# Kernel tuning notes

Measured on AMD Instinct MI355X. Metric: run time of the kernel, lower is better.

Reference implementation:

```python
import jax, jax.numpy as jnp
import numpy as np

B, S, D = 4, 2048, 1024
D_K, D_V = 1024, 1024


def setup_inputs() -> dict:
    key = jax.random.key(0)
    ks = jax.random.split(key, 9)
    s = 1.0 / np.sqrt(D)
    return {
        "q_in": jax.random.normal(ks[0], (B, S, D), jnp.float32),
        "k_in": jax.random.normal(ks[1], (B, S, D), jnp.float32),
        "v_in": jax.random.normal(ks[2], (B, S, D), jnp.float32),
        "Wq": jax.random.normal(ks[3], (D, D_K), jnp.float32) * s,
        "bq": jnp.zeros((D_K,), jnp.float32),
        "Wk": jax.random.normal(ks[4], (D, D_K), jnp.float32) * s,
        "bk": jnp.zeros((D_K,), jnp.float32),
        "Wv": jax.random.normal(ks[5], (D, D_V), jnp.float32) * s,
        "bv": jnp.zeros((D_V,), jnp.float32),
    }


def reference(q_in, k_in, v_in, Wq, bq, Wk, bk, Wv, bv):
    q = jnp.einsum("bsd,dk->bsk", q_in, Wq) + bq  # [B,S,d_k]
    k = jnp.einsum("bsd,dk->bsk", k_in, Wk) + bk  # [B,S,d_k]
    v = jnp.einsum("bsd,dv->bsv", v_in, Wv) + bv  # [B,S,d_v]
    scores = jnp.einsum("bqk,bsk->bqs", q, k) / jnp.sqrt(jnp.float32(D_K))
    attn = jax.nn.softmax(scores, axis=-1)  # [B,S,S]
    return jnp.einsum("bqs,bsv->bqv", attn, v)
```

## Files before the change

kernel.cpp:

```cpp
#include <hip/hip_runtime.h>
#include <stdint.h>

#define B_  4
#define S_  2048
#define D_  1024
#define DK_ 1024
#define DV_ 1024

typedef __attribute__((ext_vector_type(8)))  short short8;
typedef __attribute__((ext_vector_type(16))) float floatx16;

#define ASYNC16(gsrc, ldst)                                                        \
  __builtin_amdgcn_global_load_lds(                                                \
      (const __attribute__((address_space(1))) unsigned int*)(gsrc),               \
      (__attribute__((address_space(3))) unsigned int*)(ldst), 16, 0, 0)

#define WAITVM(N) asm volatile("s_waitcnt vmcnt(" #N ")" ::: "memory")

__device__ __forceinline__ unsigned short f2bf(float f) {
  union { float f; uint32_t u; } v; v.f = f;
  uint32_t r = v.u + 0x7fffu + ((v.u >> 16) & 1u);
  return (unsigned short)(r >> 16);
}

__global__ __launch_bounds__(256)
void prep(const float* __restrict__ q, const float* __restrict__ k, const float* __restrict__ v,
          const float* __restrict__ W0, const float* __restrict__ W1, const float* __restrict__ W2,
          unsigned short* __restrict__ qkv, unsigned short* __restrict__ WT) {
  const int bid = blockIdx.x, tid = threadIdx.x;
  if (bid < 12288) {
    const int t  = bid >> 12;
    const int cb = bid & 4095;
    const float* in = (t == 0) ? q : (t == 1) ? k : v;
    unsigned short* o = qkv + (long)t * ((long)B_ * S_ * D_);
    const int i0 = cb * 512 + tid;
    float4 v0 = ((const float4*)in)[i0];
    float4 v1 = ((const float4*)in)[i0 + 256];
    ushort4 u0, u1;
    u0.x = f2bf(v0.x); u0.y = f2bf(v0.y); u0.z = f2bf(v0.z); u0.w = f2bf(v0.w);
    u1.x = f2bf(v1.x); u1.y = f2bf(v1.y); u1.z = f2bf(v1.z); u1.w = f2bf(v1.w);
    ((ushort4*)o)[i0] = u0;
    ((ushort4*)o)[i0 + 256] = u1;
  } else {
    const int b2 = bid - 12288;
    const int w  = b2 >> 10;
    const int tl = b2 & 1023;
    const float* in = (w == 0) ? W0 : (w == 1) ? W1 : W2;
    unsigned short* o = WT + (long)w * D_ * DK_;
    __shared__ float tile[32][33];
    const int bx = (tl & 31) * 32, by = (tl >> 5) * 32;
    const int tx = tid & 31, ty = tid >> 5;
    for (int r = ty; r < 32; r += 8)
      tile[r][tx] = in[(long)(by + r) * DK_ + bx + tx];
    __syncthreads();
    for (int r = ty; r < 32; r += 8)
      o[(long)(bx + r) * D_ + by + tx] = f2bf(tile[tx][r]);
  }
}

__device__ __forceinline__ void storeC(float* p, float v)          { *p = v; }
__device__ __forceinline__ void storeC(unsigned short* p, float v) { *p = f2bf(v); }

template <typename OutT, int NOUT, int MODE, int KSPL>
__global__ __launch_bounds__(512, 2)
void gemm_bt256(const unsigned short* __restrict__ A0, const unsigned short* __restrict__ A1,
                const unsigned short* __restrict__ A2, const unsigned short* __restrict__ Bm,
                OutT* __restrict__ C0, OutT* __restrict__ C1, OutT* __restrict__ C2,
                const float* __restrict__ b0, const float* __restrict__ b1,
                const float* __restrict__ b2, float* __restrict__ rowsum,
                int N, int K, int lda, int ldb, long sA, long sB, long sC, float scale) {
  __shared__ __align__(16) unsigned short As[3][256 * 32];
  __shared__ __align__(16) unsigned short Bs[3][256 * 32];
  __shared__ float invs[256];
  const int tid  = threadIdx.x;
  const int lane = tid & 63, wave = tid >> 6;
  const int wm = (wave >> 2) * 128;
  const int wn = (wave & 3) * 64;
  const int lm = lane & 31;
  const int hi = lane >> 5;

  const int gx = gridDim.x, gy = gridDim.y;
  const int T  = gx * gy * (int)gridDim.z;
  const int l  = blockIdx.x + gx * (blockIdx.y + gy * blockIdx.z);
  const int l2 = (l & 7) * (T >> 3) + (l >> 3);
  const int bxi = l2 % gx;
  const int byi = (l2 / gx) % gy;
  const int bzi = l2 / (gx * gy);

  const int  kh = (KSPL > 1) ? (bzi & (KSPL - 1)) : 0;
  const long zb = (KSPL > 1) ? (bzi >> 1) : bzi;
  const int m0  = byi * 256;
  const int n0g = bxi * 256;

  const unsigned short* A = A0;
  OutT* C = C0;
  const float* bias = b0;
  int n0 = n0g, sel = 0;
  if (NOUT == 3) {
    sel = n0g >> 10;
    n0 = n0g & 1023;
    if (sel == 1)      { A = A1; C = C1; bias = b1; }
    else if (sel == 2) { A = A2; C = C2; bias = b2; }
  }
  A += zb * sA + (long)kh * K;
  const unsigned short* Bp = Bm + zb * sB + (long)kh * K;
  C += zb * sC;

  const int rr = lane >> 2;
  const int cc = (((lane & 3) ^ ((lane >> 3) & 3)) * 8);
  const unsigned short* gA0 = A  + (long)(m0  + 32 * wave + rr) * lda + cc;
  const unsigned short* gA1 = gA0 + 16 * (long)lda;
  const unsigned short* gB0 = Bp + (long)(n0g + 32 * wave + rr) * ldb + cc;
  const unsigned short* gB1 = gB0 + 16 * (long)ldb;
  const int la0 = wave * 1024, la1 = wave * 1024 + 512;

  floatx16 acc[4][2] = {};
  const int sw = (lm >> 1) & 3;

  const int nt = K >> 5;

  ASYNC16(gA0, &As[0][la0]); ASYNC16(gA1, &As[0][la1]);
  ASYNC16(gB0, &Bs[0][la0]); ASYNC16(gB1, &Bs[0][la1]);
  gA0 += 32; gA1 += 32; gB0 += 32; gB1 += 32;
  ASYNC16(gA0, &As[1][la0]); ASYNC16(gA1, &As[1][la1]);
  ASYNC16(gB0, &Bs[1][la0]); ASYNC16(gB1, &Bs[1][la1]);
  gA0 += 32; gA1 += 32; gB0 += 32; gB1 += 32;
  WAITVM(4);
  __builtin_amdgcn_s_barrier();

  int bc = 0;
  for (int t = 0; t < nt; t++) {
    const int bs = (bc + 2 >= 3) ? bc - 1 : bc + 2;
    const bool pre = (t + 2 < nt);

    short8 af[2][2], bf[2][2];
#pragma unroll
    for (int i = 0; i < 2; i++)
#pragma unroll
      for (int s = 0; s < 2; s++)
        af[i][s] = *(const short8*)&As[bc][(wm + i * 32 + lm) * 32 + (((s * 2 + hi) ^ sw) * 8)];
#pragma unroll
    for (int j = 0; j < 2; j++)
#pragma unroll
      for (int s = 0; s < 2; s++)
        bf[j][s] = *(const short8*)&Bs[bc][(wn + j * 32 + lm) * 32 + (((s * 2 + hi) ^ sw) * 8)];
    if (pre) {
      ASYNC16(gA0, &As[bs][la0]); ASYNC16(gA1, &As[bs][la1]);
      gA0 += 32; gA1 += 32;
    }
    __builtin_amdgcn_s_barrier();
    asm volatile("s_waitcnt lgkmcnt(0)" ::: "memory");
    __builtin_amdgcn_s_setprio(1);
#pragma unroll
    for (int s = 0; s < 2; s++)
#pragma unroll
      for (int i = 0; i < 2; i++)
#pragma unroll
        for (int j = 0; j < 2; j++)
          acc[i][j] = __builtin_amdgcn_mfma_f32_32x32x16_bf16(af[i][s], bf[j][s], acc[i][j], 0, 0, 0);
    __builtin_amdgcn_s_setprio(0);
    __builtin_amdgcn_s_barrier();

    short8 af2[2][2];
#pragma unroll
    for (int i = 0; i < 2; i++)
#pragma unroll
      for (int s = 0; s < 2; s++)
        af2[i][s] = *(const short8*)&As[bc][(wm + (2 + i) * 32 + lm) * 32 + (((s * 2 + hi) ^ sw) * 8)];
    if (pre) {
      ASYNC16(gB0, &Bs[bs][la0]); ASYNC16(gB1, &Bs[bs][la1]);
      gB0 += 32; gB1 += 32;
    }
    __builtin_amdgcn_s_barrier();
    asm volatile("s_waitcnt lgkmcnt(0)" ::: "memory");
    __builtin_amdgcn_s_setprio(1);
#pragma unroll
    for (int s = 0; s < 2; s++)
#pragma unroll
      for (int i = 0; i < 2; i++)
#pragma unroll
        for (int j = 0; j < 2; j++)
          acc[2 + i][j] = __builtin_amdgcn_mfma_f32_32x32x16_bf16(af2[i][s], bf[j][s], acc[2 + i][j], 0, 0, 0);
    __builtin_amdgcn_s_setprio(0);
    if (pre) { WAITVM(4); } else { WAITVM(0); }
    __builtin_amdgcn_s_barrier();
    bc = (bc == 2) ? 0 : bc + 1;
  }

  if (MODE == 2 || MODE == 3) {
    __syncthreads();
    if (tid < 256) invs[tid] = 1.0f / rowsum[zb * S_ + m0 + tid];
    __syncthreads();
  }

  if (NOUT == 3 && sel == 2) {
    unsigned short* Vt = (unsigned short*)C;
    const int b = m0 >> 11;
    const int sbase = (m0 & 2047);
#pragma unroll
    for (int i = 0; i < 4; i++) {
      const int srowb = sbase + wm + i * 32 + (hi << 2);
#pragma unroll
      for (int j = 0; j < 2; j++) {
        const int col = n0 + wn + j * 32 + lm;
        const float bv = bias[col];
        unsigned short* vp = Vt + ((long)b * DV_ + col) * S_ + srowb;
#pragma unroll
        for (int g = 0; g < 4; g++) {
          ushort4 u;
          u.x = f2bf(acc[i][j][4 * g + 0] + bv);
          u.y = f2bf(acc[i][j][4 * g + 1] + bv);
          u.z = f2bf(acc[i][j][4 * g + 2] + bv);
          u.w = f2bf(acc[i][j][4 * g + 3] + bv);
          *(ushort4*)(vp + 8 * g) = u;
        }
      }
    }
  } else if (MODE == 1) {
#pragma unroll
    for (int i = 0; i < 4; i++) {
#pragma unroll
      for (int r = 0; r < 16; r++) {
        const int row = m0 + wm + i * 32 + (r & 3) + ((r >> 2) << 3) + (hi << 2);
        float sum2 = 0.f;
#pragma unroll
        for (int j = 0; j < 2; j++) {
          const int col = n0 + wn + j * 32 + lm;
          float e = __expf(acc[i][j][r] * scale);
          storeC(C + (long)row * N + col, e);
          sum2 += e;
        }
#pragma unroll
        for (int msk = 1; msk < 32; msk <<= 1) sum2 += __shfl_xor(sum2, msk, 64);
        if ((lane & 31) == 0) atomicAdd(&rowsum[zb * S_ + row], sum2);
      }
    }
  } else {
#pragma unroll
    for (int i = 0; i < 4; i++) {
#pragma unroll
      for (int j = 0; j < 2; j++) {
        const int col = n0 + wn + j * 32 + lm;
        const float bv = bias ? bias[col] : 0.f;
#pragma unroll
        for (int r = 0; r < 16; r++) {
          const int rl = wm + i * 32 + (r & 3) + ((r >> 2) << 3) + (hi << 2);
          float val = acc[i][j][r] * scale + bv;
          if (MODE == 3) {
            atomicAdd((float*)(C + (long)(m0 + rl) * N + col), val * invs[rl]);
          } else {
            if (MODE == 2) val *= invs[rl];
            storeC(C + (long)(m0 + rl) * N + col, val);
          }
        }
      }
    }
  }
}

extern "C" void kernel_launch(void* const* d_in, const int* in_sizes, int n_in,
                              void* d_out, int out_size, void* d_ws, size_t ws_size,
                              hipStream_t stream) {
  const float* q_in = (const float*)d_in[0];
  const float* k_in = (const float*)d_in[1];
  const float* v_in = (const float*)d_in[2];
  const float* Wq   = (const float*)d_in[3];
  const float* bq   = (const float*)d_in[4];
  const float* Wk   = (const float*)d_in[5];
  const float* bk   = (const float*)d_in[6];
  const float* Wv   = (const float*)d_in[7];
  const float* bv   = (const float*)d_in[8];
  float* out = (float*)d_out;

  char* ws = (char*)d_ws;
  const long nX = (long)B_ * S_ * D_;
  const long nW = (long)D_ * DK_;
  unsigned short* qb  = (unsigned short*)(ws);
  unsigned short* kb  = qb + nX;
  unsigned short* vb  = kb + nX;
  unsigned short* WqT = vb + nX;
  unsigned short* Qb  = WqT + 3 * nW;
  unsigned short* Kb  = Qb + nX;
  unsigned short* Vt  = Kb + nX;
  float*          rowsum = (float*)(Vt + nX);
  unsigned short* U   = (unsigned short*)ws;

  dim3 blk(256), blk5(512);

  hipMemsetAsync(rowsum, 0, (size_t)B_ * S_ * sizeof(float), stream);
  hipMemsetAsync(out, 0, (size_t)B_ * S_ * DV_ * sizeof(float), stream);

  {
    dim3 g(12288 + 3072);
    prep<<<g, blk, 0, stream>>>(q_in, k_in, v_in, Wq, Wk, Wv, qb, WqT);
  }
  {
    dim3 g(3 * DK_ / 256, (B_ * S_) / 256, 1);
    gemm_bt256<unsigned short, 3, 0, 1><<<g, blk5, 0, stream>>>(
        qb, kb, vb, WqT, Qb, Kb, Vt, bq, bk, bv, nullptr,
        DK_, D_, D_, D_, 0, 0, 0, 1.f);
  }
  {
    dim3 g(S_ / 256, S_ / 256, B_);
    gemm_bt256<unsigned short, 1, 1, 1><<<g, blk5, 0, stream>>>(
        Qb, nullptr, nullptr, Kb, U, nullptr, nullptr, nullptr, nullptr, nullptr, rowsum,
        S_, DK_, DK_, DK_, (long)S_ * DK_, (long)S_ * DK_, (long)S_ * S_, 0.03125f);
  }
  {
    dim3 g(DV_ / 256, S_ / 256, B_ * 2);
    gemm_bt256<float, 1, 3, 2><<<g, blk5, 0, stream>>>(
        U, nullptr, nullptr, Vt, out, nullptr, nullptr, nullptr, nullptr, nullptr, rowsum,
        DV_, S_ / 2, S_, S_, (long)S_ * S_, (long)DV_ * S_, (long)S_ * DV_, 1.f);
  }
}
```

Before: 374.0 us.

## Replace atomic row sums and split-K atomics with separate reduction and combine kernels

The QK^T kernel no longer uses shuffle reductions and atomicAdd to build softmax row sums. A separate kernel now computes the sums from the stored bf16 exponentials. The split-K PV GEMM writes its two halves to separate buffers with plain stores instead of float atomics into a zeroed output. A combine kernel then adds the halves and normalizes by the row sum. This removes two memsets and atomic traffic, but adds two extra launches, extra passes over U and the output, and the row sums are now computed from bf16-rounded values.

```diff
diff --git a/kernel.cpp b/kernel.cpp
--- a/kernel.cpp
+++ b/kernel.cpp
@@ -21,6 +21,11 @@
   union { float f; uint32_t u; } v; v.f = f;
   uint32_t r = v.u + 0x7fffu + ((v.u >> 16) & 1u);
   return (unsigned short)(r >> 16);
+}
+
+__device__ __forceinline__ float bf2f(unsigned short u) {
+  union { uint32_t u; float f; } v; v.u = ((uint32_t)u) << 16;
+  return v.f;
 }
 
 __global__ __launch_bounds__(256)
@@ -61,17 +66,46 @@
 __device__ __forceinline__ void storeC(float* p, float v)          { *p = v; }
 __device__ __forceinline__ void storeC(unsigned short* p, float v) { *p = f2bf(v); }
 
+__global__ __launch_bounds__(256)
+void rowsumk(const unsigned short* __restrict__ U, float* __restrict__ rowsum) {
+  const int w    = (blockIdx.x << 2) + (threadIdx.x >> 6);
+  const int lane = threadIdx.x & 63;
+  const unsigned short* row = U + (long)w * S_;
+  float s = 0.f;
+#pragma unroll
+  for (int it = 0; it < 4; it++) {
+    short8 v = *(const short8*)(row + it * 512 + lane * 8);
+#pragma unroll
+    for (int e = 0; e < 8; e++) s += bf2f((unsigned short)v[e]);
+  }
+#pragma unroll
+  for (int m = 1; m < 64; m <<= 1) s += __shfl_xor(s, m, 64);
+  if (lane == 0) rowsum[w] = s;
+}
+
+__global__ __launch_bounds__(256)
+void combine(float* __restrict__ out, const float* __restrict__ P,
+             const float* __restrict__ rowsum) {
+  const long k = (long)blockIdx.x * 256 + threadIdx.x;
+  float4 a = ((const float4*)out)[k];
+  float4 b = ((const float4*)P)[k];
+  const float inv = 1.0f / rowsum[k >> 8];
+  float4 o;
+  o.x = (a.x + b.x) * inv; o.y = (a.y + b.y) * inv;
+  o.z = (a.z + b.z) * inv; o.w = (a.w + b.w) * inv;
+  ((float4*)out)[k] = o;
+}
+
 template <typename OutT, int NOUT, int MODE, int KSPL>
 __global__ __launch_bounds__(512, 2)
 void gemm_bt256(const unsigned short* __restrict__ A0, const unsigned short* __restrict__ A1,
                 const unsigned short* __restrict__ A2, const unsigned short* __restrict__ Bm,
                 OutT* __restrict__ C0, OutT* __restrict__ C1, OutT* __restrict__ C2,
                 const float* __restrict__ b0, const float* __restrict__ b1,
-                const float* __restrict__ b2, float* __restrict__ rowsum,
+                const float* __restrict__ b2,
                 int N, int K, int lda, int ldb, long sA, long sB, long sC, float scale) {
   __shared__ __align__(16) unsigned short As[3][256 * 32];
   __shared__ __align__(16) unsigned short Bs[3][256 * 32];
-  __shared__ float invs[256];
   const int tid  = threadIdx.x;
   const int lane = tid & 63, wave = tid >> 6;
   const int wm = (wave >> 2) * 128;
@@ -102,6 +136,7 @@
     if (sel == 1)      { A = A1; C = C1; bias = b1; }
     else if (sel == 2) { A = A2; C = C2; bias = b2; }
   }
+  if (KSPL > 1 && kh) C = C1;
   A += zb * sA + (long)kh * K;
   const unsigned short* Bp = Bm + zb * sB + (long)kh * K;
   C += zb * sC;
@@ -185,12 +220,6 @@
     if (pre) { WAITVM(4); } else { WAITVM(0); }
     __builtin_amdgcn_s_barrier();
     bc = (bc == 2) ? 0 : bc + 1;
-  }
-
-  if (MODE == 2 || MODE == 3) {
-    __syncthreads();
-    if (tid < 256) invs[tid] = 1.0f / rowsum[zb * S_ + m0 + tid];
-    __syncthreads();
   }
 
   if (NOUT == 3 && sel == 2) {
@@ -220,19 +249,13 @@
 #pragma unroll
     for (int i = 0; i < 4; i++) {
 #pragma unroll
-      for (int r = 0; r < 16; r++) {
-        const int row = m0 + wm + i * 32 + (r & 3) + ((r >> 2) << 3) + (hi << 2);
-        float sum2 = 0.f;
-#pragma unroll
-        for (int j = 0; j < 2; j++) {
-          const int col = n0 + wn + j * 32 + lm;
-          float e = __expf(acc[i][j][r] * scale);
-          storeC(C + (long)row * N + col, e);
-          sum2 += e;
+      for (int j = 0; j < 2; j++) {
+        const int col = n0 + wn + j * 32 + lm;
+#pragma unroll
+        for (int r = 0; r < 16; r++) {
+          const int row = m0 + wm + i * 32 + (r & 3) + ((r >> 2) << 3) + (hi << 2);
+          storeC(C + (long)row * N + col, __expf(acc[i][j][r] * scale));
         }
-#pragma unroll
-        for (int msk = 1; msk < 32; msk <<= 1) sum2 += __shfl_xor(sum2, msk, 64);
-        if ((lane & 31) == 0) atomicAdd(&rowsum[zb * S_ + row], sum2);
       }
     }
   } else {
@@ -245,13 +268,7 @@
 #pragma unroll
         for (int r = 0; r < 16; r++) {
           const int rl = wm + i * 32 + (r & 3) + ((r >> 2) << 3) + (hi << 2);
-          float val = acc[i][j][r] * scale + bv;
-          if (MODE == 3) {
-            atomicAdd((float*)(C + (long)(m0 + rl) * N + col), val * invs[rl]);
-          } else {
-            if (MODE == 2) val *= invs[rl];
-            storeC(C + (long)(m0 + rl) * N + col, val);
-          }
+          storeC(C + (long)(m0 + rl) * N + col, acc[i][j][r] * scale + bv);
         }
       }
     }
@@ -284,11 +301,9 @@
   unsigned short* Vt  = Kb + nX;
   float*          rowsum = (float*)(Vt + nX);
   unsigned short* U   = (unsigned short*)ws;
+  float*          P   = (float*)Qb;
 
   dim3 blk(256), blk5(512);
-
-  hipMemsetAsync(rowsum, 0, (size_t)B_ * S_ * sizeof(float), stream);
-  hipMemsetAsync(out, 0, (size_t)B_ * S_ * DV_ * sizeof(float), stream);
 
   {
     dim3 g(12288 + 3072);
@@ -297,19 +312,27 @@
   {
     dim3 g(3 * DK_ / 256, (B_ * S_) / 256, 1);
     gemm_bt256<unsigned short, 3, 0, 1><<<g, blk5, 0, stream>>>(
-        qb, kb, vb, WqT, Qb, Kb, Vt, bq, bk, bv, nullptr,
+        qb, kb, vb, WqT, Qb, Kb, Vt, bq, bk, bv,
         DK_, D_, D_, D_, 0, 0, 0, 1.f);
   }
   {
     dim3 g(S_ / 256, S_ / 256, B_);
     gemm_bt256<unsigned short, 1, 1, 1><<<g, blk5, 0, stream>>>(
-        Qb, nullptr, nullptr, Kb, U, nullptr, nullptr, nullptr, nullptr, nullptr, rowsum,
+        Qb, nullptr, nullptr, Kb, U, nullptr, nullptr, nullptr, nullptr, nullptr,
         S_, DK_, DK_, DK_, (long)S_ * DK_, (long)S_ * DK_, (long)S_ * S_, 0.03125f);
   }
   {
+    dim3 g((B_ * S_) / 4);
+    rowsumk<<<g, blk, 0, stream>>>(U, rowsum);
+  }
+  {
     dim3 g(DV_ / 256, S_ / 256, B_ * 2);
-    gemm_bt256<float, 1, 3, 2><<<g, blk5, 0, stream>>>(
-        U, nullptr, nullptr, Vt, out, nullptr, nullptr, nullptr, nullptr, nullptr, rowsum,
+    gemm_bt256<float, 1, 0, 2><<<g, blk5, 0, stream>>>(
+        U, nullptr, nullptr, Vt, out, P, nullptr, nullptr, nullptr, nullptr,
         DV_, S_ / 2, S_, S_, (long)S_ * S_, (long)DV_ * S_, (long)S_ * DV_, 1.f);
   }
-}
+  {
+    dim3 g((B_ * S_ * DV_) / 4 / 256);
+    combine<<<g, blk, 0, stream>>>(out, P, rowsum);
+  }
+}
```

Result: faster. 340.4 us (-9.0%).

## Replace atomics with partial buffers plus combine kernel, deepen LDS pipeline to four stages

Applied to the files above, without the earlier changes.

The softmax row sums are now written as per-column-block partials instead of atomically added, and the split-K PV GEMM writes its two halves to separate buffers (out and P) with plain stores instead of float atomics. A new combine kernel adds the halves, reduces the partial row sums and applies the normalisation. This removes both memsets and the atomic traffic. The GEMM pipeline also grows from three to four LDS buffers with deeper prefetch, which raises LDS use and may lower occupancy, and the extra combine pass rereads the output.

```diff
diff --git a/kernel.cpp b/kernel.cpp
--- a/kernel.cpp
+++ b/kernel.cpp
@@ -61,17 +61,39 @@
 __device__ __forceinline__ void storeC(float* p, float v)          { *p = v; }
 __device__ __forceinline__ void storeC(unsigned short* p, float v) { *p = f2bf(v); }
 
+__global__ __launch_bounds__(256)
+void combine(float* __restrict__ out, const float* __restrict__ P,
+             const float* __restrict__ rsp) {
+  __shared__ float sinv;
+  const int row = blockIdx.x;
+  const int tid = threadIdx.x;
+  if (tid < 32) {
+    float s = rsp[(long)tid * (B_ * S_) + row];
+#pragma unroll
+    for (int m = 1; m < 32; m <<= 1) s += __shfl_xor(s, m, 64);
+    if (tid == 0) sinv = 1.0f / s;
+  }
+  __syncthreads();
+  const float inv = sinv;
+  const long k = (long)row * 256 + tid;
+  float4 a = ((const float4*)out)[k];
+  float4 b = ((const float4*)P)[k];
+  float4 o;
+  o.x = (a.x + b.x) * inv; o.y = (a.y + b.y) * inv;
+  o.z = (a.z + b.z) * inv; o.w = (a.w + b.w) * inv;
+  ((float4*)out)[k] = o;
+}
+
 template <typename OutT, int NOUT, int MODE, int KSPL>
 __global__ __launch_bounds__(512, 2)
 void gemm_bt256(const unsigned short* __restrict__ A0, const unsigned short* __restrict__ A1,
                 const unsigned short* __restrict__ A2, const unsigned short* __restrict__ Bm,
                 OutT* __restrict__ C0, OutT* __restrict__ C1, OutT* __restrict__ C2,
                 const float* __restrict__ b0, const float* __restrict__ b1,
-                const float* __restrict__ b2, float* __restrict__ rowsum,
+                const float* __restrict__ b2, float* __restrict__ rsp,
                 int N, int K, int lda, int ldb, long sA, long sB, long sC, float scale) {
-  __shared__ __align__(16) unsigned short As[3][256 * 32];
-  __shared__ __align__(16) unsigned short Bs[3][256 * 32];
-  __shared__ float invs[256];
+  __shared__ __align__(16) unsigned short As[4][256 * 32];
+  __shared__ __align__(16) unsigned short Bs[4][256 * 32];
   const int tid  = threadIdx.x;
   const int lane = tid & 63, wave = tid >> 6;
   const int wm = (wave >> 2) * 128;
@@ -102,6 +124,7 @@
     if (sel == 1)      { A = A1; C = C1; bias = b1; }
     else if (sel == 2) { A = A2; C = C2; bias = b2; }
   }
+  if (KSPL > 1 && kh) C = C1;
   A += zb * sA + (long)kh * K;
   const unsigned short* Bp = Bm + zb * sB + (long)kh * K;
   C += zb * sC;
@@ -119,19 +142,19 @@
 
   const int nt = K >> 5;
 
-  ASYNC16(gA0, &As[0][la0]); ASYNC16(gA1, &As[0][la1]);
-  ASYNC16(gB0, &Bs[0][la0]); ASYNC16(gB1, &Bs[0][la1]);
-  gA0 += 32; gA1 += 32; gB0 += 32; gB1 += 32;
-  ASYNC16(gA0, &As[1][la0]); ASYNC16(gA1, &As[1][la1]);
-  ASYNC16(gB0, &Bs[1][la0]); ASYNC16(gB1, &Bs[1][la1]);
-  gA0 += 32; gA1 += 32; gB0 += 32; gB1 += 32;
-  WAITVM(4);
+#pragma unroll
+  for (int pt = 0; pt < 3; pt++) {
+    ASYNC16(gA0, &As[pt][la0]); ASYNC16(gA1, &As[pt][la1]);
+    ASYNC16(gB0, &Bs[pt][la0]); ASYNC16(gB1, &Bs[pt][la1]);
+    gA0 += 32; gA1 += 32; gB0 += 32; gB1 += 32;
+  }
+  WAITVM(8);
   __builtin_amdgcn_s_barrier();
 
-  int bc = 0;
   for (int t = 0; t < nt; t++) {
-    const int bs = (bc + 2 >= 3) ? bc - 1 : bc + 2;
-    const bool pre = (t + 2 < nt);
+    const int bc = t & 3;
+    const int bs = (t + 3) & 3;
+    const bool pre = (t + 3 < nt);
 
     short8 af[2][2], bf[2][2];
 #pragma unroll
@@ -182,15 +205,10 @@
         for (int j = 0; j < 2; j++)
           acc[2 + i][j] = __builtin_amdgcn_mfma_f32_32x32x16_bf16(af2[i][s], bf[j][s], acc[2 + i][j], 0, 0, 0);
     __builtin_amdgcn_s_setprio(0);
-    if (pre) { WAITVM(4); } else { WAITVM(0); }
+    if (t + 3 < nt)      { WAITVM(8); }
+    else if (t + 2 < nt) { WAITVM(4); }
+    else                 { WAITVM(0); }
     __builtin_amdgcn_s_barrier();
-    bc = (bc == 2) ? 0 : bc + 1;
-  }
-
-  if (MODE == 2 || MODE == 3) {
-    __syncthreads();
-    if (tid < 256) invs[tid] = 1.0f / rowsum[zb * S_ + m0 + tid];
-    __syncthreads();
   }
 
   if (NOUT == 3 && sel == 2) {
@@ -232,7 +250,8 @@
         }
 #pragma unroll
         for (int msk = 1; msk < 32; msk <<= 1) sum2 += __shfl_xor(sum2, msk, 64);
-        if ((lane & 31) == 0) atomicAdd(&rowsum[zb * S_ + row], sum2);
+        if ((lane & 31) == 0)
+          rsp[(long)(bxi * 4 + (wave & 3)) * (B_ * S_) + zb * S_ + row] = sum2;
       }
     }
   } else {
@@ -245,13 +264,7 @@
 #pragma unroll
         for (int r = 0; r < 16; r++) {
           const int rl = wm + i * 32 + (r & 3) + ((r >> 2) << 3) + (hi << 2);
-          float val = acc[i][j][r] * scale + bv;
-          if (MODE == 3) {
-            atomicAdd((float*)(C + (long)(m0 + rl) * N + col), val * invs[rl]);
-          } else {
-            if (MODE == 2) val *= invs[rl];
-            storeC(C + (long)(m0 + rl) * N + col, val);
-          }
+          storeC(C + (long)(m0 + rl) * N + col, acc[i][j][r] * scale + bv);
         }
       }
     }
@@ -282,13 +295,11 @@
   unsigned short* Qb  = WqT + 3 * nW;
   unsigned short* Kb  = Qb + nX;
   unsigned short* Vt  = Kb + nX;
-  float*          rowsum = (float*)(Vt + nX);
   unsigned short* U   = (unsigned short*)ws;
+  float*          rowsumP = (float*)vb;
+  float*          P   = (float*)Qb;
 
   dim3 blk(256), blk5(512);
-
-  hipMemsetAsync(rowsum, 0, (size_t)B_ * S_ * sizeof(float), stream);
-  hipMemsetAsync(out, 0, (size_t)B_ * S_ * DV_ * sizeof(float), stream);
 
   {
     dim3 g(12288 + 3072);
@@ -303,13 +314,17 @@
   {
     dim3 g(S_ / 256, S_ / 256, B_);
     gemm_bt256<unsigned short, 1, 1, 1><<<g, blk5, 0, stream>>>(
-        Qb, nullptr, nullptr, Kb, U, nullptr, nullptr, nullptr, nullptr, nullptr, rowsum,
+        Qb, nullptr, nullptr, Kb, U, nullptr, nullptr, nullptr, nullptr, nullptr, rowsumP,
         S_, DK_, DK_, DK_, (long)S_ * DK_, (long)S_ * DK_, (long)S_ * S_, 0.03125f);
   }
   {
     dim3 g(DV_ / 256, S_ / 256, B_ * 2);
-    gemm_bt256<float, 1, 3, 2><<<g, blk5, 0, stream>>>(
-        U, nullptr, nullptr, Vt, out, nullptr, nullptr, nullptr, nullptr, nullptr, rowsum,
+    gemm_bt256<float, 1, 0, 2><<<g, blk5, 0, stream>>>(
+        U, nullptr, nullptr, Vt, out, P, nullptr, nullptr, nullptr, nullptr, nullptr,
         DV_, S_ / 2, S_, S_, (long)S_ * S_, (long)DV_ * S_, (long)S_ * DV_, 1.f);
   }
-}
+  {
+    dim3 g(B_ * S_);
+    combine<<<g, blk, 0, stream>>>(out, P, rowsumP);
+  }
+}
```

Result: faster. 342.0 us (-8.6%).
